# Kernel tuning notes

Measured on AMD Instinct MI355X. Metric: run time of the kernel, lower is better.

## Reference

```python
import jax, jax.numpy as jnp
import numpy as np

B, D, VOCAB = 8192, 256, 1000000


def setup_inputs() -> dict:
    key = jax.random.key(0)
    k1, k2, k3, k4 = jax.random.split(key, 4)
    input_emb = jax.random.normal(k1, (B, D), dtype=jnp.float32)
    target_emb = jax.random.normal(k2, (B, D), dtype=jnp.float32)
    target_ids = jax.random.randint(k3, (B, 1), 0, VOCAB, dtype=jnp.int64)
    # sampling probabilities must lie strictly in (0,1)
    q_probas = jax.random.uniform(k4, (B,), dtype=jnp.float32) * 0.98 + 0.01
    return {"input_emb": input_emb, "target_emb": target_emb,
            "target_ids": target_ids, "q_probas": q_probas}


def reference(input_emb, target_emb, target_ids, q_probas):
    # sim: [B, B] in-batch similarity
    sim = input_emb @ target_emb.T
    n = q_probas.shape[0]
    # miss[i, j] = True where target j is a valid negative for row i
    miss = target_ids != target_ids.T                      # [B, B] bool
    n_miss = jnp.sum(miss, axis=1, keepdims=True).astype(sim.dtype)  # [B, 1]
    pos_sim = jnp.diagonal(sim)                            # [B]
    # logQ correction: log(n_miss * q_j / (1 - q_i)), broadcast to [B, B]
    correction = jnp.log(n_miss * q_probas[None, :] / (1.0 - q_probas[:, None]))
    mask = miss & (~jnp.eye(n, dtype=bool))                # exclude diagonal
    neg_exp = jnp.where(mask, jnp.exp(sim - correction), 0.0)  # [B, B]
    pos_exp = jnp.exp(pos_sim)
    batch_loss = jnp.mean(-pos_sim + jnp.log(pos_exp + jnp.sum(neg_exp, axis=1)))
    return batch_loss
```

## Files before the change

kernel.cpp:

```cpp
#include <hip/hip_runtime.h>
#include <hip/hip_bf16.h>
#include <stdint.h>

#define MB 8192
#define KD 256
#define BM 128
#define BN 64
#define NSPLIT 8
#define SLAB (MB / NSPLIT)
#define NCHUNK (SLAB / BN)
#define COFF 104.0f
#define LOG2E 1.44269504088896340736f

typedef __attribute__((ext_vector_type(8))) short bf16x8;
typedef __attribute__((ext_vector_type(4))) float f32x4;

__device__ __forceinline__ unsigned short f2bf(float x) {
  union { float f; uint32_t u; } v; v.f = x;
  uint32_t r = v.u + 0x7fffu + ((v.u >> 16) & 1u);
  return (unsigned short)(r >> 16);
}

__device__ __forceinline__ float fast_exp2(float x) {
#if __has_builtin(__builtin_amdgcn_exp2f)
  return __builtin_amdgcn_exp2f(x);
#else
  return exp2f(x);
#endif
}

#define GLOAD_LDS16(g, l)                                                      \
  __builtin_amdgcn_global_load_lds(                                            \
      (const __attribute__((address_space(1))) void*)(g),                      \
      (__attribute__((address_space(3))) void*)(l), 16, 0, 0)

__global__ __launch_bounds__(256) void prep_kernel(
    const float* __restrict__ A, const float* __restrict__ B,
    const float* __restrict__ q,
    unsigned short* __restrict__ Abf, unsigned short* __restrict__ Bbf,
    float* __restrict__ pos, float* __restrict__ b2,
    float* __restrict__ ps, float* __restrict__ cnt,
    float* __restrict__ out) {
  int t = blockIdx.x * 256 + threadIdx.x;
  const float4 a = ((const float4*)A)[t];
  const float4 b = ((const float4*)B)[t];
  ushort4 oa, ob;
  oa.x = f2bf(a.x); oa.y = f2bf(a.y); oa.z = f2bf(a.z); oa.w = f2bf(a.w);
  ob.x = f2bf(b.x); ob.y = f2bf(b.y); ob.z = f2bf(b.z); ob.w = f2bf(b.w);
  ((ushort4*)Abf)[t] = oa;
  ((ushort4*)Bbf)[t] = ob;
  float d = a.x * b.x + a.y * b.y + a.z * b.z + a.w * b.w;
  #pragma unroll
  for (int off = 32; off; off >>= 1) d += __shfl_down(d, off, 64);
  if ((threadIdx.x & 63) == 0) pos[t >> 6] = d;
  if (t < MB) {
    b2[t] = -(log2f(q[t]) + COFF * LOG2E);
    ps[t] = 0.0f;
    cnt[t] = 0.0f;
    if (t == 0) out[0] = 0.0f;
  }
}

__global__ __launch_bounds__(256, 2) void fused_kernel(
    const unsigned short* __restrict__ Abf,
    const unsigned short* __restrict__ Bbf,
    const int* __restrict__ ids,
    const float* __restrict__ b2,
    float* __restrict__ ps, float* __restrict__ cnt) {
  const int slab = blockIdx.y;
  const int tid = threadIdx.x;
  const int wave = tid >> 6;
  const int lane = tid & 63;
  const int quad = lane >> 4;
  const int lpos = lane & 15;
  const int rowbase = blockIdx.x * BM + wave * 32;
  const int colbase = slab * SLAB;

  __shared__ unsigned short Bs[2][2048 * 8];

  bf16x8 afrag[2][8];
  #pragma unroll
  for (int rt = 0; rt < 2; ++rt)
    #pragma unroll
    for (int kb = 0; kb < 8; ++kb)
      afrag[rt][kb] = *(const bf16x8*)(Abf + (rowbase + rt * 16 + lpos) * KD + kb * 32 + quad * 8);

  const unsigned short* gsrc[8];
  int ldso[8];
  #pragma unroll
  for (int s8 = 0; s8 < 8; ++s8) {
    int c = tid + s8 * 256;
    int lp = c & 15, qd = (c >> 4) & 3, kb = (c >> 6) & 7, ct = c >> 9;
    gsrc[s8] = Bbf + (colbase + ct * 16 + lp) * KD + kb * 32 + qd * 8;
    ldso[s8] = c * 8;
  }

  int idr[2][4];
  float srun[2][4];
  float crun[2][4];
  #pragma unroll
  for (int rt = 0; rt < 2; ++rt)
    #pragma unroll
    for (int r = 0; r < 4; ++r) {
      idr[rt][r] = ids[rowbase + rt * 16 + quad * 4 + r];
      srun[rt][r] = 0.0f;
      crun[rt][r] = 0.0f;
    }

  int idv[2][4];
  float bv[2][4];
  #pragma unroll
  for (int ct = 0; ct < 4; ++ct) {
    idv[0][ct] = ids[colbase + ct * 16 + lpos];
    bv[0][ct]  = b2 [colbase + ct * 16 + lpos];
  }
  #pragma unroll
  for (int s8 = 0; s8 < 8; ++s8)
    GLOAD_LDS16(gsrc[s8], &Bs[0][0] + ldso[s8]);
  __syncthreads();

#define FUSED_BODY(T, CUR)                                                     \
  {                                                                            \
    const int nxt = (T) + 1;                                                   \
    if (nxt < NCHUNK) {                                                        \
      _Pragma("unroll")                                                        \
      for (int ct = 0; ct < 4; ++ct) {                                         \
        idv[(CUR) ^ 1][ct] = ids[colbase + nxt * BN + ct * 16 + lpos];         \
        bv[(CUR) ^ 1][ct]  = b2 [colbase + nxt * BN + ct * 16 + lpos];         \
      }                                                                        \
      _Pragma("unroll")                                                        \
      for (int s8 = 0; s8 < 8; ++s8)                                           \
        GLOAD_LDS16(gsrc[s8] + nxt * (BN * KD), &Bs[(CUR) ^ 1][0] + ldso[s8]); \
    }                                                                          \
    _Pragma("unroll")                                                          \
    for (int ct = 0; ct < 4; ++ct) {                                           \
      const unsigned short* bp = &Bs[CUR][0] + (ct * 512 + quad * 16 + lpos) * 8; \
      bf16x8 bfrag[8];                                                         \
      _Pragma("unroll")                                                        \
      for (int kb = 0; kb < 8; ++kb)                                           \
        bfrag[kb] = *(const bf16x8*)(bp + kb * 512);                           \
      const int idj = idv[CUR][ct];                                            \
      const float bj = bv[CUR][ct];                                            \
      _Pragma("unroll")                                                        \
      for (int rt = 0; rt < 2; ++rt) {                                         \
        f32x4 acc = {0.0f, 0.0f, 0.0f, 0.0f};                                  \
        _Pragma("unroll")                                                      \
        for (int kb = 0; kb < 8; ++kb)                                         \
          acc = __builtin_amdgcn_mfma_f32_16x16x32_bf16(afrag[rt][kb], bfrag[kb], acc, 0, 0, 0); \
        _Pragma("unroll")                                                      \
        for (int r = 0; r < 4; ++r) {                                          \
          const bool eq = (idj == idr[rt][r]);                                 \
          const float e = fast_exp2(__builtin_fmaf(acc[r], LOG2E, bj));        \
          srun[rt][r] += eq ? 0.0f : e;                                        \
          crun[rt][r] += eq ? 1.0f : 0.0f;                                     \
        }                                                                      \
      }                                                                        \
    }                                                                          \
    __syncthreads();                                                           \
  }

  for (int t2 = 0; t2 < NCHUNK; t2 += 2) {
    FUSED_BODY(t2, 0)
    FUSED_BODY(t2 + 1, 1)
  }
#undef FUSED_BODY

  #pragma unroll
  for (int rt = 0; rt < 2; ++rt)
    #pragma unroll
    for (int r = 0; r < 4; ++r) {
      float v = srun[rt][r];
      float c = crun[rt][r];
      #pragma unroll
      for (int off = 1; off < 16; off <<= 1) {
        v += __shfl_xor(v, off, 64);
        c += __shfl_xor(c, off, 64);
      }
      if (lpos == 0) {
        atomicAdd(&ps[rowbase + rt * 16 + quad * 4 + r], v);
        atomicAdd(&cnt[rowbase + rt * 16 + quad * 4 + r], c);
      }
    }
}

__global__ __launch_bounds__(256) void finalize_kernel(
    const float* __restrict__ ps, const float* __restrict__ pos,
    const float* __restrict__ q, const float* __restrict__ cnt,
    float* __restrict__ out) {
  int i = blockIdx.x * 256 + threadIdx.x;
  const float s = ps[i];
  const float nm = (float)MB - cnt[i];
  const float z = logf(s) + COFF + logf(1.0f - q[i]) - logf(nm);
  const float p = pos[i];
  const float hi = fmaxf(p, z), lo = fminf(p, z);
  float loss = -p + hi + log1pf(__expf(lo - hi));

  #pragma unroll
  for (int off = 32; off; off >>= 1) loss += __shfl_down(loss, off, 64);
  __shared__ float red[4];
  if ((threadIdx.x & 63) == 0) red[threadIdx.x >> 6] = loss;
  __syncthreads();
  if (threadIdx.x == 0) {
    float t = red[0] + red[1] + red[2] + red[3];
    atomicAdd(out, t * (1.0f / (float)MB));
  }
}

extern "C" void kernel_launch(void* const* d_in, const int* in_sizes, int n_in,
                              void* d_out, int out_size, void* d_ws, size_t ws_size,
                              hipStream_t stream) {
  (void)in_sizes; (void)n_in; (void)out_size; (void)ws_size;
  const float* input_emb  = (const float*)d_in[0];
  const float* target_emb = (const float*)d_in[1];
  const int*   target_ids = (const int*)d_in[2];
  const float* q_probas   = (const float*)d_in[3];
  float* out = (float*)d_out;

  char* ws = (char*)d_ws;
  unsigned short* Abf = (unsigned short*)(ws);
  unsigned short* Bbf = (unsigned short*)(ws + (4u << 20));
  float* b2   = (float*)(ws + (8u << 20));
  float* pos  = (float*)(ws + (8u << 20) + 32768);
  float* ps   = (float*)(ws + (8u << 20) + 65536);
  float* cnt  = (float*)(ws + (8u << 20) + 98304);

  prep_kernel<<<2048, 256, 0, stream>>>(input_emb, target_emb, q_probas,
                                        Abf, Bbf, pos, b2, ps, cnt, out);
  fused_kernel<<<dim3(MB / BM, NSPLIT), 256, 0, stream>>>(Abf, Bbf, target_ids,
                                                          b2, ps, cnt);
  finalize_kernel<<<32, 256, 0, stream>>>(ps, pos, q_probas, cnt, out);
}
```

Measured before the change: 119.8 us.

## Stage slab ids/bias in LDS and use partial vmcnt waits for prefetch overlap

Loads the whole slab's target ids and bias values into shared memory once at kernel start, replacing per-chunk global loads into registers. It also replaces __syncthreads with explicit s_waitcnt vmcnt(8) plus raw s_barrier, so the next chunk's B tile prefetch stays in flight while the current chunk computes. The aim is to cut global-load latency stalls and register pressure. The hand-written wait counts depend on the exact number of outstanding loads, which makes the code fragile if the load count changes.

```diff
diff --git a/kernel.cpp b/kernel.cpp
--- a/kernel.cpp
+++ b/kernel.cpp
@@ -77,6 +77,11 @@
   const int colbase = slab * SLAB;
 
   __shared__ unsigned short Bs[2][2048 * 8];
+  __shared__ int   ids_s[SLAB];
+  __shared__ float b2_s[SLAB];
+
+  const int4   tiv = ((const int4*)(ids + colbase))[tid];
+  const float4 tbv = ((const float4*)(b2 + colbase))[tid];
 
   bf16x8 afrag[2][8];
   #pragma unroll
@@ -94,6 +99,11 @@
     gsrc[s8] = Bbf + (colbase + ct * 16 + lp) * KD + kb * 32 + qd * 8;
     ldso[s8] = c * 8;
   }
+
+#define STAGE(T, BUF)                                                          \
+  _Pragma("unroll")                                                            \
+  for (int s8 = 0; s8 < 8; ++s8)                                               \
+    GLOAD_LDS16(gsrc[s8] + (T) * (BN * KD), &Bs[BUF][0] + ldso[s8]);
 
   int idr[2][4];
   float srun[2][4];
@@ -107,40 +117,32 @@
       crun[rt][r] = 0.0f;
     }
 
-  int idv[2][4];
-  float bv[2][4];
-  #pragma unroll
-  for (int ct = 0; ct < 4; ++ct) {
-    idv[0][ct] = ids[colbase + ct * 16 + lpos];
-    bv[0][ct]  = b2 [colbase + ct * 16 + lpos];
-  }
-  #pragma unroll
-  for (int s8 = 0; s8 < 8; ++s8)
-    GLOAD_LDS16(gsrc[s8], &Bs[0][0] + ldso[s8]);
+  STAGE(0, 0)
+  ((int4*)ids_s)[tid] = tiv;
+  ((float4*)b2_s)[tid] = tbv;
   __syncthreads();
 
 #define FUSED_BODY(T, CUR)                                                     \
   {                                                                            \
     const int nxt = (T) + 1;                                                   \
     if (nxt < NCHUNK) {                                                        \
-      _Pragma("unroll")                                                        \
-      for (int ct = 0; ct < 4; ++ct) {                                         \
-        idv[(CUR) ^ 1][ct] = ids[colbase + nxt * BN + ct * 16 + lpos];         \
-        bv[(CUR) ^ 1][ct]  = b2 [colbase + nxt * BN + ct * 16 + lpos];         \
-      }                                                                        \
-      _Pragma("unroll")                                                        \
-      for (int s8 = 0; s8 < 8; ++s8)                                           \
-        GLOAD_LDS16(gsrc[s8] + nxt * (BN * KD), &Bs[(CUR) ^ 1][0] + ldso[s8]); \
+      STAGE(nxt, (CUR) ^ 1)                                                    \
+      asm volatile("s_waitcnt vmcnt(8)" ::: "memory");                         \
+    } else {                                                                   \
+      asm volatile("s_waitcnt vmcnt(0)" ::: "memory");                         \
     }                                                                          \
+    __builtin_amdgcn_s_barrier();              \
+    __builtin_amdgcn_sched_barrier(0);                                         \
     _Pragma("unroll")                                                          \
     for (int ct = 0; ct < 4; ++ct) {                                           \
+      const int jloc = (T) * BN + ct * 16 + lpos;                              \
+      const int idj = ids_s[jloc];                                             \
+      const float bj = b2_s[jloc];                                             \
       const unsigned short* bp = &Bs[CUR][0] + (ct * 512 + quad * 16 + lpos) * 8; \
       bf16x8 bfrag[8];                                                         \
       _Pragma("unroll")                                                        \
       for (int kb = 0; kb < 8; ++kb)                                           \
         bfrag[kb] = *(const bf16x8*)(bp + kb * 512);                           \
-      const int idj = idv[CUR][ct];                                            \
-      const float bj = bv[CUR][ct];                                            \
       _Pragma("unroll")                                                        \
       for (int rt = 0; rt < 2; ++rt) {                                         \
         f32x4 acc = {0.0f, 0.0f, 0.0f, 0.0f};                                  \
@@ -156,7 +158,9 @@
         }                                                                      \
       }                                                                        \
     }                                                                          \
-    __syncthreads();                                                           \
+    asm volatile("" ::: "memory");                                             \
+    __builtin_amdgcn_s_barrier();             \
+    __builtin_amdgcn_sched_barrier(0);        \
   }
 
   for (int t2 = 0; t2 < NCHUNK; t2 += 2) {
@@ -164,6 +168,7 @@
     FUSED_BODY(t2 + 1, 1)
   }
 #undef FUSED_BODY
+#undef STAGE
 
   #pragma unroll
   for (int rt = 0; rt < 2; ++rt)
```

New measurement: 115.6 us. 3.4% less time.
